# Optimization experiments

Hardware: AMD Instinct MI355X
Metric: run time of the kernel (lower is better)

The kernel has to match this reference:

```python
import jax, jax.numpy as jnp
import numpy as np

N_E, N_C, H = 100000, 50000, 256
D_E, D_C = 768, 1024
E_EE, E_EC, E_CE = 800000, 400000, 400000
EPS = 1e-12


def setup_inputs() -> dict:
    key = jax.random.key(0)
    ks = jax.random.split(key, 16)
    x_entity = jax.random.normal(ks[0], (N_E, D_E), jnp.float32)
    x_chunk = jax.random.normal(ks[1], (N_C, D_C), jnp.float32)
    # edge[0] = source indices, edge[1] = destination indices
    edge_ee = jnp.stack([jax.random.randint(ks[2], (E_EE,), 0, N_E),
                         jax.random.randint(ks[3], (E_EE,), 0, N_E)])
    edge_ec = jnp.stack([jax.random.randint(ks[4], (E_EC,), 0, N_E),
                         jax.random.randint(ks[5], (E_EC,), 0, N_C)])
    edge_ce = jnp.stack([jax.random.randint(ks[6], (E_CE,), 0, N_C),
                         jax.random.randint(ks[7], (E_CE,), 0, N_E)])
    # per-type projection weights (stored [in, out]; y = x @ W)
    P_e = jax.random.normal(ks[8], (D_E, H), jnp.float32) / np.sqrt(D_E).astype(np.float32)
    P_c = jax.random.normal(ks[9], (D_C, H), jnp.float32) / np.sqrt(D_C).astype(np.float32)
    s = np.float32(1.0 / np.sqrt(H))
    # SAGEConv params stacked over the 3 edge types: 0=e->e, 1=e->c, 2=c->e
    Wl1 = jax.random.normal(ks[10], (3, H, H), jnp.float32) * s
    bl1 = jnp.zeros((3, H), jnp.float32)
    Wr1 = jax.random.normal(ks[11], (3, H, H), jnp.float32) * s
    Wl2 = jax.random.normal(ks[12], (3, H, H), jnp.float32) * s
    bl2 = jnp.zeros((3, H), jnp.float32)
    Wr2 = jax.random.normal(ks[13], (3, H, H), jnp.float32) * s
    return {"x_entity": x_entity, "x_chunk": x_chunk,
            "edge_ee": edge_ee, "edge_ec": edge_ec, "edge_ce": edge_ce,
            "P_e": P_e, "P_c": P_c,
            "Wl1": Wl1, "bl1": bl1, "Wr1": Wr1,
            "Wl2": Wl2, "bl2": bl2, "Wr2": Wr2}


def _sage(x_src, x_dst, edge, Wl, bl, Wr, n_dst):
    # PyG SAGEConv: lin_l(mean of neighbor features) + lin_r(x_dst)
    msg = x_src[edge[0]]                                   # [E, H] gather
    agg = jax.ops.segment_sum(msg, edge[1], num_segments=n_dst)
    cnt = jax.ops.segment_sum(jnp.ones((edge.shape[1], 1), x_src.dtype),
                              edge[1], num_segments=n_dst)
    mean = agg / jnp.maximum(cnt, 1.0)                     # isolated nodes -> 0
    return mean @ Wl + bl + x_dst @ Wr


def _l2norm(v):
    # F.normalize(v, dim=1), eps=1e-12
    n = jnp.sqrt(jnp.sum(v * v, axis=1, keepdims=True))
    return v / jnp.maximum(n, EPS)


def reference(x_entity, x_chunk, edge_ee, edge_ec, edge_ce,
              P_e, P_c, Wl1, bl1, Wr1, Wl2, bl2, Wr2):
    # per-type projection (bias=False)
    h_e = x_entity @ P_e
    h_c = x_chunk @ P_c
    id_e, id_c = h_e, h_c
    # conv1: HeteroConv(aggr='sum') -> sum SAGE outputs per destination type
    o_e = (_sage(h_e, h_e, edge_ee, Wl1[0], bl1[0], Wr1[0], N_E)
           + _sage(h_c, h_e, edge_ce, Wl1[2], bl1[2], Wr1[2], N_E))
    o_c = _sage(h_e, h_c, edge_ec, Wl1[1], bl1[1], Wr1[1], N_C)
    # dropout(0.1) is identity in eval; relu then residual
    h_e = jax.nn.relu(o_e) + id_e
    h_c = jax.nn.relu(o_c) + id_c
    # conv2
    o_e = (_sage(h_e, h_e, edge_ee, Wl2[0], bl2[0], Wr2[0], N_E)
           + _sage(h_c, h_e, edge_ce, Wl2[2], bl2[2], Wr2[2], N_E))
    o_c = _sage(h_e, h_c, edge_ec, Wl2[1], bl2[1], Wr2[1], N_C)
    return _l2norm(o_e), _l2norm(o_c)
```

## Files before the change

kernel.cpp:

```cpp
#include <hip/hip_runtime.h>
#include <hip/hip_bf16.h>

#define N_E 100000
#define N_C 50000
#define H 256
#define D_E 768
#define D_C 1024
#define E_EE 800000
#define E_EC 400000
#define E_CE 400000

#define ME_PAD 100096
#define MC_PAD 50048

typedef unsigned short u16;
typedef __attribute__((ext_vector_type(8))) short bf16x8;
typedef __attribute__((ext_vector_type(4))) float f32x4;

__device__ __forceinline__ float bf2f(u16 x) {
    unsigned u = ((unsigned)x) << 16;
    return __builtin_bit_cast(float, u);
}
__device__ __forceinline__ u16 f2bf(float f) {
    unsigned u = __builtin_bit_cast(unsigned, f);
    u = (u + 0x7fffu + ((u >> 16) & 1u)) >> 16;
    return (u16)u;
}

__global__ __launch_bounds__(1024) void transpose_w_k(const float* __restrict__ in,
                                                      u16* __restrict__ out, int K) {
    __shared__ float t[32][33];
    int k0 = blockIdx.x * 32, n0 = blockIdx.y * 32;
    int tx = threadIdx.x, ty = threadIdx.y;
    t[ty][tx] = in[(size_t)(k0 + ty) * H + n0 + tx];
    __syncthreads();
    out[(size_t)(n0 + ty) * K + k0 + tx] = f2bf(t[tx][ty]);
}

__global__ __launch_bounds__(1024) void transpose_wsum_k(const float* __restrict__ a,
                                                         const float* __restrict__ b,
                                                         u16* __restrict__ out) {
    __shared__ float t[32][33];
    int k0 = blockIdx.x * 32, n0 = blockIdx.y * 32;
    int tx = threadIdx.x, ty = threadIdx.y;
    size_t idx = (size_t)(k0 + ty) * H + n0 + tx;
    t[ty][tx] = a[idx] + b[idx];
    __syncthreads();
    out[(size_t)(n0 + ty) * H + k0 + tx] = f2bf(t[tx][ty]);
}

__global__ __launch_bounds__(256) void hist_k(const int* __restrict__ dst, int E,
                                              int* __restrict__ cnt) {
    int i = blockIdx.x * 256 + threadIdx.x;
    if (i < E) atomicAdd(&cnt[dst[i]], 1);
}

#define SCAN_N (2 * N_E + N_C)
#define SCAN_NB ((SCAN_N + 1023) / 1024)

__global__ __launch_bounds__(1024) void scan_blk_k(const int* __restrict__ cnt,
                                                   int* __restrict__ part,
                                                   int* __restrict__ bsum) {
    __shared__ int sm[1024];
    int i = blockIdx.x * 1024 + threadIdx.x;
    int v = (i < SCAN_N) ? cnt[i] : 0;
    sm[threadIdx.x] = v;
    __syncthreads();
    for (int off = 1; off < 1024; off <<= 1) {
        int t = (threadIdx.x >= off) ? sm[threadIdx.x - off] : 0;
        __syncthreads();
        sm[threadIdx.x] += t;
        __syncthreads();
    }
    if (i < SCAN_N) part[i] = sm[threadIdx.x] - v;
    if (threadIdx.x == 1023) bsum[blockIdx.x] = sm[1023];
}

__global__ __launch_bounds__(1024) void scan_top_k(int* __restrict__ bsum) {
    __shared__ int sm[1024];
    int v = (threadIdx.x < SCAN_NB) ? bsum[threadIdx.x] : 0;
    sm[threadIdx.x] = v;
    __syncthreads();
    for (int off = 1; off < 1024; off <<= 1) {
        int t = (threadIdx.x >= off) ? sm[threadIdx.x - off] : 0;
        __syncthreads();
        sm[threadIdx.x] += t;
        __syncthreads();
    }
    if (threadIdx.x < SCAN_NB) bsum[threadIdx.x] = sm[threadIdx.x] - v;
}

__global__ __launch_bounds__(1024) void scan_out_k(const int* __restrict__ part,
                                                   const int* __restrict__ bsum,
                                                   int* __restrict__ eePtr, int* __restrict__ eeCur,
                                                   int* __restrict__ cePtr, int* __restrict__ ceCur,
                                                   int* __restrict__ ecPtr, int* __restrict__ ecCur) {
    int i = blockIdx.x * 1024 + threadIdx.x;
    if (i < SCAN_N) {
        int v = part[i] + bsum[blockIdx.x];
        if (i < N_E) {
            eePtr[i] = v; eeCur[i] = v;
        } else if (i < 2 * N_E) {
            int j = i - N_E, w = v - E_EE;
            cePtr[j] = w; ceCur[j] = w;
        } else {
            int j = i - 2 * N_E, w = v - (E_EE + E_CE);
            ecPtr[j] = w; ecCur[j] = w;
        }
    }
    if (i == 0) {
        eePtr[N_E] = E_EE;
        cePtr[N_E] = E_CE;
        ecPtr[N_C] = E_EC;
    }
}

__global__ __launch_bounds__(256) void reorder_k(const int* __restrict__ src,
                                                 const int* __restrict__ dst, int E,
                                                 int* __restrict__ cursor,
                                                 int* __restrict__ srcSorted) {
    int e = blockIdx.x * 256 + threadIdx.x;
    if (e < E) {
        int pos = atomicAdd(&cursor[dst[e]], 1);
        srcSorted[pos] = src[e];
    }
}

__global__ __launch_bounds__(256) void gather_mean_k(const u16* __restrict__ feat,
                                                     const int* __restrict__ rowptr,
                                                     const int* __restrict__ srcIdx,
                                                     int nDst, int nPad,
                                                     u16* __restrict__ outAgg) {
    int r = blockIdx.x * 4 + (threadIdx.x >> 6);
    if (r >= nPad) return;
    int lane = threadIdx.x & 63;
    float ax = 0.f, ay = 0.f, az = 0.f, aw = 0.f;
    int deg = 0;
    if (r < nDst) {
        int e0 = rowptr[r], e1 = rowptr[r + 1];
        deg = e1 - e0;
        int e = e0;
        for (; e + 1 < e1; e += 2) {
            int s0 = srcIdx[e], s1 = srcIdx[e + 1];
            ushort4 v0 = *reinterpret_cast<const ushort4*>(feat + (size_t)s0 * H + lane * 4);
            ushort4 v1 = *reinterpret_cast<const ushort4*>(feat + (size_t)s1 * H + lane * 4);
            ax += bf2f(v0.x) + bf2f(v1.x);
            ay += bf2f(v0.y) + bf2f(v1.y);
            az += bf2f(v0.z) + bf2f(v1.z);
            aw += bf2f(v0.w) + bf2f(v1.w);
        }
        if (e < e1) {
            int s0 = srcIdx[e];
            ushort4 v0 = *reinterpret_cast<const ushort4*>(feat + (size_t)s0 * H + lane * 4);
            ax += bf2f(v0.x); ay += bf2f(v0.y); az += bf2f(v0.z); aw += bf2f(v0.w);
        }
    }
    float inv = deg > 0 ? 1.f / (float)deg : 0.f;
    ushort4 o;
    o.x = f2bf(ax * inv); o.y = f2bf(ay * inv); o.z = f2bf(az * inv); o.w = f2bf(aw * inv);
    *reinterpret_cast<ushort4*>(outAgg + (size_t)r * H + lane * 4) = o;
}


struct GemmArgs {
    const u16* A[3];
    const u16* Wt[3];
    int K;
    int nPairs;
    const float* bias1;
    const float* bias2;
    const u16* res;
    void* out;
    int Mvalid;
    int mode;
};

__global__ __launch_bounds__(512, 4) void gemm_bf16_k(GemmArgs g) {
    __shared__ char lds[2][24576];
    __shared__ float rowsq[128];
    const int tid = threadIdx.x;
    const int lane = tid & 63;
    const int wid = tid >> 6;
    const int wm = wid >> 2;
    const int wn = wid & 3;
    const int row0 = blockIdx.x * 128;
    const int K = g.K;

    const int srow = tid >> 2;
    const int au = (tid & 3) ^ ((srow >> 1) & 3);
    const int ofsA = (row0 + srow) * K + au * 8;
    const int ofsB1 = srow * K + au * 8;
    const int brow2 = 128 + srow;
    const int bu2 = (tid & 3) ^ ((brow2 >> 1) & 3);
    const int ofsB2 = brow2 * K + bu2 * 8;

    int a_off[4], b_off[4];
#pragma unroll
    for (int mi = 0; mi < 4; ++mi) {
        int row = wm * 64 + mi * 16 + (lane & 15);
        int u = (lane >> 4) ^ ((row >> 1) & 3);
        a_off[mi] = row * 64 + u * 16;
    }
#pragma unroll
    for (int ni = 0; ni < 4; ++ni) {
        int row = wn * 64 + ni * 16 + (lane & 15);
        int u = (lane >> 4) ^ ((row >> 1) & 3);
        b_off[ni] = 8192 + row * 64 + u * 16;
    }

#define STAGE(p_, kk_, ph_)                                                                       \
    do {                                                                                          \
        const u16* A_ = g.A[p_];                                                                  \
        const u16* W_ = g.Wt[p_];                                                                 \
        __builtin_amdgcn_global_load_lds(                                                         \
            (const __attribute__((address_space(1))) void*)(A_ + ofsA + (kk_)),                   \
            (__attribute__((address_space(3))) void*)(lds[ph_] + wid * 1024), 16, 0, 0);          \
        __builtin_amdgcn_global_load_lds(                                                         \
            (const __attribute__((address_space(1))) void*)(W_ + ofsB1 + (kk_)),                  \
            (__attribute__((address_space(3))) void*)(lds[ph_] + 8192 + wid * 1024), 16, 0, 0);   \
        __builtin_amdgcn_global_load_lds(                                                         \
            (const __attribute__((address_space(1))) void*)(W_ + ofsB2 + (kk_)),                  \
            (__attribute__((address_space(3))) void*)(lds[ph_] + 16384 + wid * 1024), 16, 0, 0);  \
    } while (0)

    f32x4 acc[4][4] = {};
    const int T = g.nPairs * (K >> 5);

    STAGE(0, 0, 0);
    int pn = 0, kn = 32;
    if (kn == K) { kn = 0; pn = 1; }

    for (int s = 0; s < T; ++s) {
        const int ph = s & 1;
        if (s + 1 < T) {
            STAGE(pn, kn, ph ^ 1);
            kn += 32;
            if (kn == K) { kn = 0; ++pn; }
            asm volatile("s_waitcnt vmcnt(3)" ::: "memory");
        } else {
            asm volatile("s_waitcnt vmcnt(0)" ::: "memory");
        }
        __builtin_amdgcn_sched_barrier(0);
        __builtin_amdgcn_s_barrier();

        bf16x8 af[4], bfr[4];
#pragma unroll
        for (int mi = 0; mi < 4; ++mi)
            af[mi] = *reinterpret_cast<const bf16x8*>(lds[ph] + a_off[mi]);
#pragma unroll
        for (int ni = 0; ni < 4; ++ni)
            bfr[ni] = *reinterpret_cast<const bf16x8*>(lds[ph] + b_off[ni]);
#pragma unroll
        for (int mi = 0; mi < 4; ++mi)
#pragma unroll
            for (int ni = 0; ni < 4; ++ni)
                acc[mi][ni] = __builtin_amdgcn_mfma_f32_16x16x32_bf16(af[mi], bfr[ni],
                                                                      acc[mi][ni], 0, 0, 0);
        __builtin_amdgcn_sched_barrier(0);
        __builtin_amdgcn_s_barrier();
    }
#undef STAGE

    const int ccol = wn * 64 + (lane & 15);
    const int crow0 = row0 + wm * 64 + ((lane >> 4) << 2);
    float bv[4];
#pragma unroll
    for (int ni = 0; ni < 4; ++ni) {
        int c = ccol + ni * 16;
        float b = 0.f;
        if (g.bias1) b += g.bias1[c];
        if (g.bias2) b += g.bias2[c];
        bv[ni] = b;
    }

    if (g.mode == 1) {
#pragma unroll
        for (int ni = 0; ni < 4; ++ni) {
            int c = ccol + ni * 16;
#pragma unroll
            for (int mi = 0; mi < 4; ++mi) {
#pragma unroll
                for (int j = 0; j < 4; ++j) {
                    int r = crow0 + mi * 16 + j;
                    size_t idx = (size_t)r * H + c;
                    float v = fmaxf(acc[mi][ni][j] + bv[ni], 0.f) + bf2f(g.res[idx]);
                    ((u16*)g.out)[idx] = f2bf(v);
                }
            }
        }
    } else {
        if (tid < 128) rowsq[tid] = 0.f;
        __syncthreads();
#pragma unroll
        for (int mi = 0; mi < 4; ++mi) {
#pragma unroll
            for (int j = 0; j < 4; ++j) {
                float p = 0.f;
#pragma unroll
                for (int ni = 0; ni < 4; ++ni) {
                    float v = acc[mi][ni][j] + bv[ni];
                    p += v * v;
                }
                p += __shfl_xor(p, 1);
                p += __shfl_xor(p, 2);
                p += __shfl_xor(p, 4);
                p += __shfl_xor(p, 8);
                if ((lane & 15) == 0) {
                    int rl = wm * 64 + mi * 16 + ((lane >> 4) << 2) + j;
                    atomicAdd(&rowsq[rl], p);
                }
            }
        }
        __syncthreads();
#pragma unroll
        for (int mi = 0; mi < 4; ++mi) {
#pragma unroll
            for (int j = 0; j < 4; ++j) {
                int rl = wm * 64 + mi * 16 + ((lane >> 4) << 2) + j;
                int r = row0 + rl;
                if (r < g.Mvalid) {
                    float inv = 1.f / fmaxf(sqrtf(rowsq[rl]), 1e-12f);
#pragma unroll
                    for (int ni = 0; ni < 4; ++ni) {
                        int c = ccol + ni * 16;
                        float v = acc[mi][ni][j] + bv[ni];
                        ((float*)g.out)[(size_t)r * H + c] = v * inv;
                    }
                }
            }
        }
    }
}

struct ProjArgs {
    const float* A;
    const u16* Wt;
    int K;
    int M;
    u16* out;
};

__global__ __launch_bounds__(512, 4) void gemm_proj_k(ProjArgs g) {
    __shared__ char lds[2][24576];
    const int tid = threadIdx.x;
    const int lane = tid & 63;
    const int wid = tid >> 6;
    const int wm = wid >> 2;
    const int wn = wid & 3;
    const int row0 = blockIdx.x * 128;
    const int K = g.K;

    const int srow = tid >> 2;
    const int cunit = tid & 3;
    const int aRow = min(row0 + srow, g.M - 1);
    const float* pA = g.A + (size_t)aRow * K + cunit * 8;
    const int aDst = srow * 64 + (cunit ^ ((srow >> 1) & 3)) * 16;

    const int bu1 = cunit ^ ((srow >> 1) & 3);
    const int ofsB1 = srow * K + bu1 * 8;
    const int brow2 = 128 + srow;
    const int bu2 = cunit ^ ((brow2 >> 1) & 3);
    const int ofsB2 = brow2 * K + bu2 * 8;

    int a_off[4], b_off[4];
#pragma unroll
    for (int mi = 0; mi < 4; ++mi) {
        int row = wm * 64 + mi * 16 + (lane & 15);
        int u = (lane >> 4) ^ ((row >> 1) & 3);
        a_off[mi] = row * 64 + u * 16;
    }
#pragma unroll
    for (int ni = 0; ni < 4; ++ni) {
        int row = wn * 64 + ni * 16 + (lane & 15);
        int u = (lane >> 4) ^ ((row >> 1) & 3);
        b_off[ni] = 8192 + row * 64 + u * 16;
    }

#define BSTAGE(kk_, ph_)                                                                          \
    do {                                                                                          \
        __builtin_amdgcn_global_load_lds(                                                         \
            (const __attribute__((address_space(1))) void*)(g.Wt + ofsB1 + (kk_)),               \
            (__attribute__((address_space(3))) void*)(lds[ph_] + 8192 + wid * 1024), 16, 0, 0);   \
        __builtin_amdgcn_global_load_lds(                                                         \
            (const __attribute__((address_space(1))) void*)(g.Wt + ofsB2 + (kk_)),               \
            (__attribute__((address_space(3))) void*)(lds[ph_] + 16384 + wid * 1024), 16, 0, 0);  \
    } while (0)

    f32x4 acc[4][4] = {};
    const int T = K >> 5;

    BSTAGE(0, 0);
    float4 c0 = *reinterpret_cast<const float4*>(pA);
    float4 c1 = *reinterpret_cast<const float4*>(pA + 4);

    for (int s = 0; s < T; ++s) {
        const int ph = s & 1;
        float4 n0 = make_float4(0.f, 0.f, 0.f, 0.f), n1 = n0;
        if (s + 1 < T) {
            BSTAGE((s + 1) * 32, ph ^ 1);
            n0 = *reinterpret_cast<const float4*>(pA + (s + 1) * 32);
            n1 = *reinterpret_cast<const float4*>(pA + (s + 1) * 32 + 4);
        }
        union { bf16x8 v; u16 e[8]; } pk;
        pk.e[0] = f2bf(c0.x); pk.e[1] = f2bf(c0.y); pk.e[2] = f2bf(c0.z); pk.e[3] = f2bf(c0.w);
        pk.e[4] = f2bf(c1.x); pk.e[5] = f2bf(c1.y); pk.e[6] = f2bf(c1.z); pk.e[7] = f2bf(c1.w);
        *reinterpret_cast<bf16x8*>(lds[ph] + aDst) = pk.v;
        asm volatile("s_waitcnt lgkmcnt(0)" ::: "memory");
        __builtin_amdgcn_sched_barrier(0);
        __builtin_amdgcn_s_barrier();

        bf16x8 af[4], bfr[4];
#pragma unroll
        for (int mi = 0; mi < 4; ++mi)
            af[mi] = *reinterpret_cast<const bf16x8*>(lds[ph] + a_off[mi]);
#pragma unroll
        for (int ni = 0; ni < 4; ++ni)
            bfr[ni] = *reinterpret_cast<const bf16x8*>(lds[ph] + b_off[ni]);
#pragma unroll
        for (int mi = 0; mi < 4; ++mi)
#pragma unroll
            for (int ni = 0; ni < 4; ++ni)
                acc[mi][ni] = __builtin_amdgcn_mfma_f32_16x16x32_bf16(af[mi], bfr[ni],
                                                                      acc[mi][ni], 0, 0, 0);
        __builtin_amdgcn_sched_barrier(0);
        __builtin_amdgcn_s_barrier();
        c0 = n0; c1 = n1;
    }
#undef BSTAGE

    const int ccol = wn * 64 + (lane & 15);
    const int crow0 = row0 + wm * 64 + ((lane >> 4) << 2);
#pragma unroll
    for (int ni = 0; ni < 4; ++ni) {
        int c = ccol + ni * 16;
#pragma unroll
        for (int mi = 0; mi < 4; ++mi) {
#pragma unroll
            for (int j = 0; j < 4; ++j) {
                int r = crow0 + mi * 16 + j;
                g.out[(size_t)r * H + c] = f2bf(acc[mi][ni][j]);
            }
        }
    }
}

extern "C" void kernel_launch(void* const* d_in, const int* in_sizes, int n_in,
                              void* d_out, int out_size, void* d_ws, size_t ws_size,
                              hipStream_t stream) {
    const float* x_e = (const float*)d_in[0];
    const float* x_c = (const float*)d_in[1];
    const int* e_ee = (const int*)d_in[2];
    const int* e_ec = (const int*)d_in[3];
    const int* e_ce = (const int*)d_in[4];
    const float* P_e = (const float*)d_in[5];
    const float* P_c = (const float*)d_in[6];
    const float* Wl1 = (const float*)d_in[7];
    const float* bl1 = (const float*)d_in[8];
    const float* Wr1 = (const float*)d_in[9];
    const float* Wl2 = (const float*)d_in[10];
    const float* bl2 = (const float*)d_in[11];
    const float* Wr2 = (const float*)d_in[12];
    float* out = (float*)d_out;

    const size_t EHp = (size_t)ME_PAD * H;
    const size_t CHp = (size_t)MC_PAD * H;

    u16* us = (u16*)d_ws;
    u16* he0 = us;   us += EHp;
    u16* he1 = us;   us += EHp;
    u16* aggE1 = us; us += EHp;
    u16* aggE2 = us; us += EHp;
    u16* hc0 = us;   us += CHp;
    u16* hc1 = us;   us += CHp;
    u16* aggC = us;  us += CHp;
    u16* PeT = us;   us += H * D_E;
    u16* PcT = us;   us += H * D_C;
    u16* WlT1 = us;  us += 3 * H * H;
    u16* WrT1_1 = us; us += H * H;
    u16* WrT1s = us;  us += H * H;
    u16* WlT2 = us;  us += 3 * H * H;
    u16* WrT2_1 = us; us += H * H;
    u16* WrT2s = us;  us += H * H;

    int* ip = (int*)us;
    int* eePtr = ip;  ip += N_E + 1;
    int* eeSrc = ip;  ip += E_EE;
    int* eeCur = ip;  ip += N_E;
    int* cePtr = ip;  ip += N_E + 1;
    int* ceSrc = ip;  ip += E_CE;
    int* ceCur = ip;  ip += N_E;
    int* ecPtr = ip;  ip += N_C + 1;
    int* ecSrc = ip;  ip += E_EC;
    int* ecCur = ip;  ip += N_C;
    int* cntAll = ip; ip += SCAN_N;
    int* part = ip;   ip += SCAN_N;
    int* bsum = ip;   ip += SCAN_NB + 1;

    const int WHH = H * H;

    hipMemsetAsync(cntAll, 0, (size_t)SCAN_N * sizeof(int), stream);
    hist_k<<<(E_EE + 255) / 256, 256, 0, stream>>>(e_ee + E_EE, E_EE, cntAll);
    hist_k<<<(E_CE + 255) / 256, 256, 0, stream>>>(e_ce + E_CE, E_CE, cntAll + N_E);
    hist_k<<<(E_EC + 255) / 256, 256, 0, stream>>>(e_ec + E_EC, E_EC, cntAll + 2 * N_E);
    scan_blk_k<<<SCAN_NB, 1024, 0, stream>>>(cntAll, part, bsum);
    scan_top_k<<<1, 1024, 0, stream>>>(bsum);
    scan_out_k<<<SCAN_NB, 1024, 0, stream>>>(part, bsum, eePtr, eeCur, cePtr, ceCur, ecPtr, ecCur);
    reorder_k<<<(E_EE + 255) / 256, 256, 0, stream>>>(e_ee, e_ee + E_EE, E_EE, eeCur, eeSrc);
    reorder_k<<<(E_CE + 255) / 256, 256, 0, stream>>>(e_ce, e_ce + E_CE, E_CE, ceCur, ceSrc);
    reorder_k<<<(E_EC + 255) / 256, 256, 0, stream>>>(e_ec, e_ec + E_EC, E_EC, ecCur, ecSrc);

    {
        dim3 blk(32, 32);
        transpose_w_k<<<dim3(D_E / 32, H / 32), blk, 0, stream>>>(P_e, PeT, D_E);
        transpose_w_k<<<dim3(D_C / 32, H / 32), blk, 0, stream>>>(P_c, PcT, D_C);
        for (int p = 0; p < 3; ++p) {
            transpose_w_k<<<dim3(H / 32, H / 32), blk, 0, stream>>>(Wl1 + p * WHH, WlT1 + p * WHH, H);
            transpose_w_k<<<dim3(H / 32, H / 32), blk, 0, stream>>>(Wl2 + p * WHH, WlT2 + p * WHH, H);
        }
        transpose_w_k<<<dim3(H / 32, H / 32), blk, 0, stream>>>(Wr1 + 1 * WHH, WrT1_1, H);
        transpose_w_k<<<dim3(H / 32, H / 32), blk, 0, stream>>>(Wr2 + 1 * WHH, WrT2_1, H);
        transpose_wsum_k<<<dim3(H / 32, H / 32), blk, 0, stream>>>(Wr1 + 0 * WHH, Wr1 + 2 * WHH, WrT1s);
        transpose_wsum_k<<<dim3(H / 32, H / 32), blk, 0, stream>>>(Wr2 + 0 * WHH, Wr2 + 2 * WHH, WrT2s);
    }

    const int gridE = ME_PAD / 128, gridC = MC_PAD / 128;

    {
        ProjArgs g{x_e, PeT, D_E, N_E, he0};
        gemm_proj_k<<<gridE, 512, 0, stream>>>(g);
    }
    {
        ProjArgs g{x_c, PcT, D_C, N_C, hc0};
        gemm_proj_k<<<gridC, 512, 0, stream>>>(g);
    }

    gather_mean_k<<<ME_PAD / 4, 256, 0, stream>>>(he0, eePtr, eeSrc, N_E, ME_PAD, aggE1);
    gather_mean_k<<<ME_PAD / 4, 256, 0, stream>>>(hc0, cePtr, ceSrc, N_E, ME_PAD, aggE2);
    gather_mean_k<<<MC_PAD / 4, 256, 0, stream>>>(he0, ecPtr, ecSrc, N_C, MC_PAD, aggC);
    {
        GemmArgs g{};
        g.A[0] = aggE1; g.Wt[0] = WlT1 + 0 * WHH;
        g.A[1] = aggE2; g.Wt[1] = WlT1 + 2 * WHH;
        g.A[2] = he0;   g.Wt[2] = WrT1s;
        g.K = H; g.nPairs = 3;
        g.bias1 = bl1 + 0 * H; g.bias2 = bl1 + 2 * H;
        g.res = he0; g.out = he1; g.mode = 1;
        gemm_bf16_k<<<gridE, 512, 0, stream>>>(g);
    }
    {
        GemmArgs g{};
        g.A[0] = aggC; g.Wt[0] = WlT1 + 1 * WHH;
        g.A[1] = hc0;  g.Wt[1] = WrT1_1;
        g.K = H; g.nPairs = 2;
        g.bias1 = bl1 + 1 * H;
        g.res = hc0; g.out = hc1; g.mode = 1;
        gemm_bf16_k<<<gridC, 512, 0, stream>>>(g);
    }

    gather_mean_k<<<ME_PAD / 4, 256, 0, stream>>>(he1, eePtr, eeSrc, N_E, ME_PAD, aggE1);
    gather_mean_k<<<ME_PAD / 4, 256, 0, stream>>>(hc1, cePtr, ceSrc, N_E, ME_PAD, aggE2);
    gather_mean_k<<<MC_PAD / 4, 256, 0, stream>>>(he1, ecPtr, ecSrc, N_C, MC_PAD, aggC);
    {
        GemmArgs g{};
        g.A[0] = aggE1; g.Wt[0] = WlT2 + 0 * WHH;
        g.A[1] = aggE2; g.Wt[1] = WlT2 + 2 * WHH;
        g.A[2] = he1;   g.Wt[2] = WrT2s;
        g.K = H; g.nPairs = 3;
        g.bias1 = bl2 + 0 * H; g.bias2 = bl2 + 2 * H;
        g.out = out; g.Mvalid = N_E; g.mode = 2;
        gemm_bf16_k<<<gridE, 512, 0, stream>>>(g);
    }
    {
        GemmArgs g{};
        g.A[0] = aggC; g.Wt[0] = WlT2 + 1 * WHH;
        g.A[1] = hc1;  g.Wt[1] = WrT2_1;
        g.K = H; g.nPairs = 2;
        g.bias1 = bl2 + 1 * H;
        g.out = out + (size_t)N_E * H; g.Mvalid = N_C; g.mode = 2;
        gemm_bf16_k<<<gridC, 512, 0, stream>>>(g);
    }
}
```

Measured before the change: 982.4 us.

## Batch per-edge-type kernels into single launches and widen gather loads

Merges the three histogram, reorder and gather launches, the two projection GEMMs, the paired conv GEMMs and the twelve weight transposes into one grouped launch each, with the job chosen from the block index. This cuts launch count and the tail idle time between small kernels. The gather also moves from 8-byte to 16-byte loads, with two half-wavefronts working on different edges and combining their sums through a cross-lane shuffle. Packing the indices into one combined cursor/source buffer adds some per-thread branching, and the transpose grid launches idle blocks for the smaller jobs.

New measurement: 893.4 us. 9.1% less time.

```diff
diff --git a/kernel.cpp b/kernel.cpp
--- a/kernel.cpp
+++ b/kernel.cpp
@@ -9,6 +9,7 @@
 #define E_EE 800000
 #define E_EC 400000
 #define E_CE 400000
+#define E_TOT (E_EE + E_CE + E_EC)
 
 #define ME_PAD 100096
 #define MC_PAD 50048
@@ -27,32 +28,38 @@
     return (u16)u;
 }
 
-__global__ __launch_bounds__(1024) void transpose_w_k(const float* __restrict__ in,
-                                                      u16* __restrict__ out, int K) {
-    __shared__ float t[32][33];
-    int k0 = blockIdx.x * 32, n0 = blockIdx.y * 32;
-    int tx = threadIdx.x, ty = threadIdx.y;
-    t[ty][tx] = in[(size_t)(k0 + ty) * H + n0 + tx];
-    __syncthreads();
-    out[(size_t)(n0 + ty) * K + k0 + tx] = f2bf(t[tx][ty]);
-}
-
-__global__ __launch_bounds__(1024) void transpose_wsum_k(const float* __restrict__ a,
-                                                         const float* __restrict__ b,
-                                                         u16* __restrict__ out) {
-    __shared__ float t[32][33];
-    int k0 = blockIdx.x * 32, n0 = blockIdx.y * 32;
+struct TransJobs {
+    const float* a[12];
+    const float* b[12];
+    u16* dst[12];
+    int K[12];
+};
+
+__global__ __launch_bounds__(1024) void transpose_all_k(TransJobs t) {
+    int j = blockIdx.z;
+    int K = t.K[j];
+    int k0 = blockIdx.x * 32;
+    if (k0 >= K) return;
+    int n0 = blockIdx.y * 32;
+    __shared__ float sm[32][33];
     int tx = threadIdx.x, ty = threadIdx.y;
     size_t idx = (size_t)(k0 + ty) * H + n0 + tx;
-    t[ty][tx] = a[idx] + b[idx];
+    float v = t.a[j][idx];
+    if (t.b[j]) v += t.b[j][idx];
+    sm[ty][tx] = v;
     __syncthreads();
-    out[(size_t)(n0 + ty) * H + k0 + tx] = f2bf(t[tx][ty]);
-}
-
-__global__ __launch_bounds__(256) void hist_k(const int* __restrict__ dst, int E,
-                                              int* __restrict__ cnt) {
+    t.dst[j][(size_t)(n0 + ty) * K + k0 + tx] = f2bf(sm[tx][ty]);
+}
+
+__global__ __launch_bounds__(256) void hist3_k(const int* __restrict__ eeD,
+                                               const int* __restrict__ ceD,
+                                               const int* __restrict__ ecD,
+                                               int* __restrict__ cnt) {
     int i = blockIdx.x * 256 + threadIdx.x;
-    if (i < E) atomicAdd(&cnt[dst[i]], 1);
+    if (i >= E_TOT) return;
+    if (i < E_EE) atomicAdd(&cnt[eeD[i]], 1);
+    else if (i < E_EE + E_CE) atomicAdd(&cnt[N_E + ceD[i - E_EE]], 1);
+    else atomicAdd(&cnt[2 * N_E + ecD[i - E_EE - E_CE]], 1);
 }
 
 #define SCAN_N (2 * N_E + N_C)
@@ -92,21 +99,22 @@
 
 __global__ __launch_bounds__(1024) void scan_out_k(const int* __restrict__ part,
                                                    const int* __restrict__ bsum,
-                                                   int* __restrict__ eePtr, int* __restrict__ eeCur,
-                                                   int* __restrict__ cePtr, int* __restrict__ ceCur,
-                                                   int* __restrict__ ecPtr, int* __restrict__ ecCur) {
+                                                   int* __restrict__ eePtr,
+                                                   int* __restrict__ cePtr,
+                                                   int* __restrict__ ecPtr,
+                                                   int* __restrict__ curAll) {
     int i = blockIdx.x * 1024 + threadIdx.x;
     if (i < SCAN_N) {
         int v = part[i] + bsum[blockIdx.x];
+        int w;
         if (i < N_E) {
-            eePtr[i] = v; eeCur[i] = v;
+            w = v; eePtr[i] = w;
         } else if (i < 2 * N_E) {
-            int j = i - N_E, w = v - E_EE;
-            cePtr[j] = w; ceCur[j] = w;
+            w = v - E_EE; cePtr[i - N_E] = w;
         } else {
-            int j = i - 2 * N_E, w = v - (E_EE + E_CE);
-            ecPtr[j] = w; ecCur[j] = w;
-        }
+            w = v - (E_EE + E_CE); ecPtr[i - 2 * N_E] = w;
+        }
+        curAll[i] = w;
     }
     if (i == 0) {
         eePtr[N_E] = E_EE;
@@ -115,57 +123,100 @@
     }
 }
 
-__global__ __launch_bounds__(256) void reorder_k(const int* __restrict__ src,
-                                                 const int* __restrict__ dst, int E,
-                                                 int* __restrict__ cursor,
-                                                 int* __restrict__ srcSorted) {
-    int e = blockIdx.x * 256 + threadIdx.x;
-    if (e < E) {
-        int pos = atomicAdd(&cursor[dst[e]], 1);
-        srcSorted[pos] = src[e];
-    }
-}
-
-__global__ __launch_bounds__(256) void gather_mean_k(const u16* __restrict__ feat,
-                                                     const int* __restrict__ rowptr,
-                                                     const int* __restrict__ srcIdx,
-                                                     int nDst, int nPad,
-                                                     u16* __restrict__ outAgg) {
-    int r = blockIdx.x * 4 + (threadIdx.x >> 6);
-    if (r >= nPad) return;
-    int lane = threadIdx.x & 63;
-    float ax = 0.f, ay = 0.f, az = 0.f, aw = 0.f;
+__global__ __launch_bounds__(256) void reorder3_k(const int* __restrict__ eeS, const int* __restrict__ eeD,
+                                                  const int* __restrict__ ceS, const int* __restrict__ ceD,
+                                                  const int* __restrict__ ecS, const int* __restrict__ ecD,
+                                                  int* __restrict__ curAll, int* __restrict__ srcAll) {
+    int i = blockIdx.x * 256 + threadIdx.x;
+    if (i >= E_TOT) return;
+    if (i < E_EE) {
+        int pos = atomicAdd(&curAll[eeD[i]], 1);
+        srcAll[pos] = eeS[i];
+    } else if (i < E_EE + E_CE) {
+        int k = i - E_EE;
+        int pos = atomicAdd(&curAll[N_E + ceD[k]], 1);
+        srcAll[E_EE + pos] = ceS[k];
+    } else {
+        int k = i - E_EE - E_CE;
+        int pos = atomicAdd(&curAll[2 * N_E + ecD[k]], 1);
+        srcAll[E_EE + E_CE + pos] = ecS[k];
+    }
+}
+
+struct GatherArgs {
+    const u16* feat[3];
+    const int* rowptr[3];
+    const int* srcIdx[3];
+    u16* outAgg[3];
+    int nDst[3];
+    int blkEnd[3];
+};
+
+__device__ __forceinline__ void acc8(float* a, uint4 v) {
+    a[0] += __builtin_bit_cast(float, v.x << 16);
+    a[1] += __builtin_bit_cast(float, v.x & 0xffff0000u);
+    a[2] += __builtin_bit_cast(float, v.y << 16);
+    a[3] += __builtin_bit_cast(float, v.y & 0xffff0000u);
+    a[4] += __builtin_bit_cast(float, v.z << 16);
+    a[5] += __builtin_bit_cast(float, v.z & 0xffff0000u);
+    a[6] += __builtin_bit_cast(float, v.w << 16);
+    a[7] += __builtin_bit_cast(float, v.w & 0xffff0000u);
+}
+
+__global__ __launch_bounds__(256) void gather3_k(GatherArgs a) {
+    const int b = blockIdx.x;
+    const int j = (b >= a.blkEnd[0]) + (b >= a.blkEnd[1]);
+    const int b0 = j ? a.blkEnd[j - 1] : 0;
+    const int r = (b - b0) * 4 + (threadIdx.x >> 6);
+    const int lane = threadIdx.x & 63;
+    const int half = lane >> 5;
+    const int pos = lane & 31;
+
+    float acc[8] = {};
     int deg = 0;
-    if (r < nDst) {
-        int e0 = rowptr[r], e1 = rowptr[r + 1];
+    if (r < a.nDst[j]) {
+        const int* __restrict__ rp = a.rowptr[j];
+        const int* __restrict__ si = a.srcIdx[j];
+        const u16* __restrict__ ft = a.feat[j];
+        int e0 = rp[r], e1 = rp[r + 1];
         deg = e1 - e0;
         int e = e0;
+        for (; e + 3 < e1; e += 4) {
+            int sA = si[e + half];
+            int sB = si[e + 2 + half];
+            uint4 vA = *(const uint4*)(ft + (size_t)sA * H + pos * 8);
+            uint4 vB = *(const uint4*)(ft + (size_t)sB * H + pos * 8);
+            acc8(acc, vA);
+            acc8(acc, vB);
+        }
         for (; e + 1 < e1; e += 2) {
-            int s0 = srcIdx[e], s1 = srcIdx[e + 1];
-            ushort4 v0 = *reinterpret_cast<const ushort4*>(feat + (size_t)s0 * H + lane * 4);
-            ushort4 v1 = *reinterpret_cast<const ushort4*>(feat + (size_t)s1 * H + lane * 4);
-            ax += bf2f(v0.x) + bf2f(v1.x);
-            ay += bf2f(v0.y) + bf2f(v1.y);
-            az += bf2f(v0.z) + bf2f(v1.z);
-            aw += bf2f(v0.w) + bf2f(v1.w);
-        }
-        if (e < e1) {
-            int s0 = srcIdx[e];
-            ushort4 v0 = *reinterpret_cast<const ushort4*>(feat + (size_t)s0 * H + lane * 4);
-            ax += bf2f(v0.x); ay += bf2f(v0.y); az += bf2f(v0.z); aw += bf2f(v0.w);
-        }
-    }
-    float inv = deg > 0 ? 1.f / (float)deg : 0.f;
-    ushort4 o;
-    o.x = f2bf(ax * inv); o.y = f2bf(ay * inv); o.z = f2bf(az * inv); o.w = f2bf(aw * inv);
-    *reinterpret_cast<ushort4*>(outAgg + (size_t)r * H + lane * 4) = o;
-}
-
-
-struct GemmArgs {
+            int s = si[e + half];
+            uint4 v = *(const uint4*)(ft + (size_t)s * H + pos * 8);
+            acc8(acc, v);
+        }
+        if (e < e1 && half == 0) {
+            int s = si[e];
+            uint4 v = *(const uint4*)(ft + (size_t)s * H + pos * 8);
+            acc8(acc, v);
+        }
+    }
+#pragma unroll
+    for (int k = 0; k < 8; ++k) acc[k] += __shfl_xor(acc[k], 32);
+
+    if (half == 0) {
+        float inv = deg > 0 ? 1.f / (float)deg : 0.f;
+        uint4 o;
+        o.x = (unsigned)f2bf(acc[0] * inv) | ((unsigned)f2bf(acc[1] * inv) << 16);
+        o.y = (unsigned)f2bf(acc[2] * inv) | ((unsigned)f2bf(acc[3] * inv) << 16);
+        o.z = (unsigned)f2bf(acc[4] * inv) | ((unsigned)f2bf(acc[5] * inv) << 16);
+        o.w = (unsigned)f2bf(acc[6] * inv) | ((unsigned)f2bf(acc[7] * inv) << 16);
+        *(uint4*)(a.outAgg[j] + (size_t)r * H + pos * 8) = o;
+    }
+}
+
+struct GemmCfg {
     const u16* A[3];
     const u16* Wt[3];
-    int K;
     int nPairs;
     const float* bias1;
     const float* bias2;
@@ -174,8 +225,16 @@
     int Mvalid;
     int mode;
 };
-
-__global__ __launch_bounds__(512, 4) void gemm_bf16_k(GemmArgs g) {
+struct ConvArgs2 {
+    GemmCfg c[2];
+    int blkSplit;
+};
+
+__global__ __launch_bounds__(512, 4) void gemm_conv_k(ConvArgs2 gg) {
+    const int which = blockIdx.x >= gg.blkSplit;
+    const GemmCfg* __restrict__ g = which ? &gg.c[1] : &gg.c[0];
+    const int row0 = (blockIdx.x - (which ? gg.blkSplit : 0)) * 128;
+
     __shared__ char lds[2][24576];
     __shared__ float rowsq[128];
     const int tid = threadIdx.x;
@@ -183,16 +242,14 @@
     const int wid = tid >> 6;
     const int wm = wid >> 2;
     const int wn = wid & 3;
-    const int row0 = blockIdx.x * 128;
-    const int K = g.K;
 
     const int srow = tid >> 2;
     const int au = (tid & 3) ^ ((srow >> 1) & 3);
-    const int ofsA = (row0 + srow) * K + au * 8;
-    const int ofsB1 = srow * K + au * 8;
+    const int ofsA = (row0 + srow) * H + au * 8;
+    const int ofsB1 = srow * H + au * 8;
     const int brow2 = 128 + srow;
     const int bu2 = (tid & 3) ^ ((brow2 >> 1) & 3);
-    const int ofsB2 = brow2 * K + bu2 * 8;
+    const int ofsB2 = brow2 * H + bu2 * 8;
 
     int a_off[4], b_off[4];
 #pragma unroll
@@ -210,8 +267,8 @@
 
 #define STAGE(p_, kk_, ph_)                                                                       \
     do {                                                                                          \
-        const u16* A_ = g.A[p_];                                                                  \
-        const u16* W_ = g.Wt[p_];                                                                 \
+        const u16* A_ = g->A[p_];                                                                 \
+        const u16* W_ = g->Wt[p_];                                                                \
         __builtin_amdgcn_global_load_lds(                                                         \
             (const __attribute__((address_space(1))) void*)(A_ + ofsA + (kk_)),                   \
             (__attribute__((address_space(3))) void*)(lds[ph_] + wid * 1024), 16, 0, 0);          \
@@ -224,18 +281,18 @@
     } while (0)
 
     f32x4 acc[4][4] = {};
-    const int T = g.nPairs * (K >> 5);
+    const int T = g->nPairs * (H >> 5);
 
     STAGE(0, 0, 0);
     int pn = 0, kn = 32;
-    if (kn == K) { kn = 0; pn = 1; }
+    if (kn == H) { kn = 0; pn = 1; }
 
     for (int s = 0; s < T; ++s) {
         const int ph = s & 1;
         if (s + 1 < T) {
             STAGE(pn, kn, ph ^ 1);
             kn += 32;
-            if (kn == K) { kn = 0; ++pn; }
+            if (kn == H) { kn = 0; ++pn; }
             asm volatile("s_waitcnt vmcnt(3)" ::: "memory");
         } else {
             asm volatile("s_waitcnt vmcnt(0)" ::: "memory");
@@ -268,12 +325,12 @@
     for (int ni = 0; ni < 4; ++ni) {
         int c = ccol + ni * 16;
         float b = 0.f;
-        if (g.bias1) b += g.bias1[c];
-        if (g.bias2) b += g.bias2[c];
+        if (g->bias1) b += g->bias1[c];
+        if (g->bias2) b += g->bias2[c];
         bv[ni] = b;
     }
 
-    if (g.mode == 1) {
+    if (g->mode == 1) {
 #pragma unroll
         for (int ni = 0; ni < 4; ++ni) {
             int c = ccol + ni * 16;
@@ -283,8 +340,8 @@
                 for (int j = 0; j < 4; ++j) {
                     int r = crow0 + mi * 16 + j;
                     size_t idx = (size_t)r * H + c;
-                    float v = fmaxf(acc[mi][ni][j] + bv[ni], 0.f) + bf2f(g.res[idx]);
-                    ((u16*)g.out)[idx] = f2bf(v);
+                    float v = fmaxf(acc[mi][ni][j] + bv[ni], 0.f) + bf2f(g->res[idx]);
+                    ((u16*)g->out)[idx] = f2bf(v);
                 }
             }
         }
@@ -318,13 +375,13 @@
             for (int j = 0; j < 4; ++j) {
                 int rl = wm * 64 + mi * 16 + ((lane >> 4) << 2) + j;
                 int r = row0 + rl;
-                if (r < g.Mvalid) {
+                if (r < g->Mvalid) {
                     float inv = 1.f / fmaxf(sqrtf(rowsq[rl]), 1e-12f);
 #pragma unroll
                     for (int ni = 0; ni < 4; ++ni) {
                         int c = ccol + ni * 16;
                         float v = acc[mi][ni][j] + bv[ni];
-                        ((float*)g.out)[(size_t)r * H + c] = v * inv;
+                        ((float*)g->out)[(size_t)r * H + c] = v * inv;
                     }
                 }
             }
@@ -332,28 +389,35 @@
     }
 }
 
-struct ProjArgs {
-    const float* A;
-    const u16* Wt;
-    int K;
-    int M;
-    u16* out;
+struct ProjArgs2 {
+    const float* A[2];
+    const u16* Wt[2];
+    int K[2];
+    int M[2];
+    u16* out[2];
+    int blkSplit;
 };
 
-__global__ __launch_bounds__(512, 4) void gemm_proj_k(ProjArgs g) {
+__global__ __launch_bounds__(512, 4) void gemm_proj_k(ProjArgs2 gg) {
+    const int which = blockIdx.x >= gg.blkSplit;
+    const int row0 = (blockIdx.x - (which ? gg.blkSplit : 0)) * 128;
+    const float* __restrict__ Aptr = gg.A[which];
+    const u16* __restrict__ Wt = gg.Wt[which];
+    const int K = gg.K[which];
+    const int M = gg.M[which];
+    u16* __restrict__ outp = gg.out[which];
+
     __shared__ char lds[2][24576];
     const int tid = threadIdx.x;
     const int lane = tid & 63;
     const int wid = tid >> 6;
     const int wm = wid >> 2;
     const int wn = wid & 3;
-    const int row0 = blockIdx.x * 128;
-    const int K = g.K;
 
     const int srow = tid >> 2;
     const int cunit = tid & 3;
-    const int aRow = min(row0 + srow, g.M - 1);
-    const float* pA = g.A + (size_t)aRow * K + cunit * 8;
+    const int aRow = min(row0 + srow, M - 1);
+    const float* pA = Aptr + (size_t)aRow * K + cunit * 8;
     const int aDst = srow * 64 + (cunit ^ ((srow >> 1) & 3)) * 16;
 
     const int bu1 = cunit ^ ((srow >> 1) & 3);
@@ -379,10 +443,10 @@
 #define BSTAGE(kk_, ph_)                                                                          \
     do {                                                                                          \
         __builtin_amdgcn_global_load_lds(                                                         \
-            (const __attribute__((address_space(1))) void*)(g.Wt + ofsB1 + (kk_)),               \
+            (const __attribute__((address_space(1))) void*)(Wt + ofsB1 + (kk_)),                  \
             (__attribute__((address_space(3))) void*)(lds[ph_] + 8192 + wid * 1024), 16, 0, 0);   \
         __builtin_amdgcn_global_load_lds(                                                         \
-            (const __attribute__((address_space(1))) void*)(g.Wt + ofsB2 + (kk_)),               \
+            (const __attribute__((address_space(1))) void*)(Wt + ofsB2 + (kk_)),                  \
             (__attribute__((address_space(3))) void*)(lds[ph_] + 16384 + wid * 1024), 16, 0, 0);  \
     } while (0)
 
@@ -438,7 +502,7 @@
 #pragma unroll
             for (int j = 0; j < 4; ++j) {
                 int r = crow0 + mi * 16 + j;
-                g.out[(size_t)r * H + c] = f2bf(acc[mi][ni][j]);
+                outp[(size_t)r * H + c] = f2bf(acc[mi][ni][j]);
             }
         }
     }
@@ -484,14 +548,10 @@
 
     int* ip = (int*)us;
     int* eePtr = ip;  ip += N_E + 1;
-    int* eeSrc = ip;  ip += E_EE;
-    int* eeCur = ip;  ip += N_E;
     int* cePtr = ip;  ip += N_E + 1;
-    int* ceSrc = ip;  ip += E_CE;
-    int* ceCur = ip;  ip += N_E;
     int* ecPtr = ip;  ip += N_C + 1;
-    int* ecSrc = ip;  ip += E_EC;
-    int* ecCur = ip;  ip += N_C;
+    int* curAll = ip; ip += SCAN_N;
+    int* srcAll = ip; ip += E_TOT;
     int* cntAll = ip; ip += SCAN_N;
     int* part = ip;   ip += SCAN_N;
     int* bsum = ip;   ip += SCAN_NB + 1;
@@ -499,84 +559,93 @@
     const int WHH = H * H;
 
     hipMemsetAsync(cntAll, 0, (size_t)SCAN_N * sizeof(int), stream);
-    hist_k<<<(E_EE + 255) / 256, 256, 0, stream>>>(e_ee + E_EE, E_EE, cntAll);
-    hist_k<<<(E_CE + 255) / 256, 256, 0, stream>>>(e_ce + E_CE, E_CE, cntAll + N_E);
-    hist_k<<<(E_EC + 255) / 256, 256, 0, stream>>>(e_ec + E_EC, E_EC, cntAll + 2 * N_E);
+    hist3_k<<<(E_TOT + 255) / 256, 256, 0, stream>>>(e_ee + E_EE, e_ce + E_CE, e_ec + E_EC, cntAll);
     scan_blk_k<<<SCAN_NB, 1024, 0, stream>>>(cntAll, part, bsum);
     scan_top_k<<<1, 1024, 0, stream>>>(bsum);
-    scan_out_k<<<SCAN_NB, 1024, 0, stream>>>(part, bsum, eePtr, eeCur, cePtr, ceCur, ecPtr, ecCur);
-    reorder_k<<<(E_EE + 255) / 256, 256, 0, stream>>>(e_ee, e_ee + E_EE, E_EE, eeCur, eeSrc);
-    reorder_k<<<(E_CE + 255) / 256, 256, 0, stream>>>(e_ce, e_ce + E_CE, E_CE, ceCur, ceSrc);
-    reorder_k<<<(E_EC + 255) / 256, 256, 0, stream>>>(e_ec, e_ec + E_EC, E_EC, ecCur, ecSrc);
+    scan_out_k<<<SCAN_NB, 1024, 0, stream>>>(part, bsum, eePtr, cePtr, ecPtr, curAll);
+    reorder3_k<<<(E_TOT + 255) / 256, 256, 0, stream>>>(e_ee, e_ee + E_EE, e_ce, e_ce + E_CE,
+                                                        e_ec, e_ec + E_EC, curAll, srcAll);
+    const int* eeSrc = srcAll;
+    const int* ceSrc = srcAll + E_EE;
+    const int* ecSrc = srcAll + E_EE + E_CE;
 
     {
-        dim3 blk(32, 32);
-        transpose_w_k<<<dim3(D_E / 32, H / 32), blk, 0, stream>>>(P_e, PeT, D_E);
-        transpose_w_k<<<dim3(D_C / 32, H / 32), blk, 0, stream>>>(P_c, PcT, D_C);
-        for (int p = 0; p < 3; ++p) {
-            transpose_w_k<<<dim3(H / 32, H / 32), blk, 0, stream>>>(Wl1 + p * WHH, WlT1 + p * WHH, H);
-            transpose_w_k<<<dim3(H / 32, H / 32), blk, 0, stream>>>(Wl2 + p * WHH, WlT2 + p * WHH, H);
-        }
-        transpose_w_k<<<dim3(H / 32, H / 32), blk, 0, stream>>>(Wr1 + 1 * WHH, WrT1_1, H);
-        transpose_w_k<<<dim3(H / 32, H / 32), blk, 0, stream>>>(Wr2 + 1 * WHH, WrT2_1, H);
-        transpose_wsum_k<<<dim3(H / 32, H / 32), blk, 0, stream>>>(Wr1 + 0 * WHH, Wr1 + 2 * WHH, WrT1s);
-        transpose_wsum_k<<<dim3(H / 32, H / 32), blk, 0, stream>>>(Wr2 + 0 * WHH, Wr2 + 2 * WHH, WrT2s);
+        TransJobs t{};
+        int n = 0;
+        auto add = [&](const float* a, const float* b, u16* d, int K) {
+            t.a[n] = a; t.b[n] = b; t.dst[n] = d; t.K[n] = K; ++n;
+        };
+        add(P_e, nullptr, PeT, D_E);
+        add(P_c, nullptr, PcT, D_C);
+        for (int p = 0; p < 3; ++p) add(Wl1 + p * WHH, nullptr, WlT1 + p * WHH, H);
+        for (int p = 0; p < 3; ++p) add(Wl2 + p * WHH, nullptr, WlT2 + p * WHH, H);
+        add(Wr1 + 1 * WHH, nullptr, WrT1_1, H);
+        add(Wr2 + 1 * WHH, nullptr, WrT2_1, H);
+        add(Wr1 + 0 * WHH, Wr1 + 2 * WHH, WrT1s, H);
+        add(Wr2 + 0 * WHH, Wr2 + 2 * WHH, WrT2s, H);
+        transpose_all_k<<<dim3(D_C / 32, H / 32, 12), dim3(32, 32), 0, stream>>>(t);
     }
 
     const int gridE = ME_PAD / 128, gridC = MC_PAD / 128;
 
     {
-        ProjArgs g{x_e, PeT, D_E, N_E, he0};
-        gemm_proj_k<<<gridE, 512, 0, stream>>>(g);
-    }
+        ProjArgs2 g{};
+        g.A[0] = x_e; g.Wt[0] = PeT; g.K[0] = D_E; g.M[0] = N_E; g.out[0] = he0;
+        g.A[1] = x_c; g.Wt[1] = PcT; g.K[1] = D_C; g.M[1] = N_C; g.out[1] = hc0;
+        g.blkSplit = gridE;
+        gemm_proj_k<<<gridE + gridC, 512, 0, stream>>>(g);
+    }
+
+    const int gBlkE = ME_PAD / 4, gBlkC = MC_PAD / 4;
+    const int gTotal = 2 * gBlkE + gBlkC;
+
     {
-        ProjArgs g{x_c, PcT, D_C, N_C, hc0};
-        gemm_proj_k<<<gridC, 512, 0, stream>>>(g);
-    }
-
-    gather_mean_k<<<ME_PAD / 4, 256, 0, stream>>>(he0, eePtr, eeSrc, N_E, ME_PAD, aggE1);
-    gather_mean_k<<<ME_PAD / 4, 256, 0, stream>>>(hc0, cePtr, ceSrc, N_E, ME_PAD, aggE2);
-    gather_mean_k<<<MC_PAD / 4, 256, 0, stream>>>(he0, ecPtr, ecSrc, N_C, MC_PAD, aggC);
+        GatherArgs a{};
+        a.feat[0] = he0; a.rowptr[0] = eePtr; a.srcIdx[0] = eeSrc; a.outAgg[0] = aggE1; a.nDst[0] = N_E;
+        a.feat[1] = hc0; a.rowptr[1] = cePtr; a.srcIdx[1] = ceSrc; a.outAgg[1] = aggE2; a.nDst[1] = N_E;
+        a.feat[2] = he0; a.rowptr[2] = ecPtr; a.srcIdx[2] = ecSrc; a.outAgg[2] = aggC;  a.nDst[2] = N_C;
+        a.blkEnd[0] = gBlkE; a.blkEnd[1] = 2 * gBlkE; a.blkEnd[2] = gTotal;
+        gather3_k<<<gTotal, 256, 0, stream>>>(a);
+    }
     {
-        GemmArgs g{};
-        g.A[0] = aggE1; g.Wt[0] = WlT1 + 0 * WHH;
-        g.A[1] = aggE2; g.Wt[1] = WlT1 + 2 * WHH;
-        g.A[2] = he0;   g.Wt[2] = WrT1s;
-        g.K = H; g.nPairs = 3;
-        g.bias1 = bl1 + 0 * H; g.bias2 = bl1 + 2 * H;
-        g.res = he0; g.out = he1; g.mode = 1;
-        gemm_bf16_k<<<gridE, 512, 0, stream>>>(g);
-    }
+        ConvArgs2 g{};
+        g.c[0].A[0] = aggE1; g.c[0].Wt[0] = WlT1 + 0 * WHH;
+        g.c[0].A[1] = aggE2; g.c[0].Wt[1] = WlT1 + 2 * WHH;
+        g.c[0].A[2] = he0;   g.c[0].Wt[2] = WrT1s;
+        g.c[0].nPairs = 3;
+        g.c[0].bias1 = bl1 + 0 * H; g.c[0].bias2 = bl1 + 2 * H;
+        g.c[0].res = he0; g.c[0].out = he1; g.c[0].mode = 1;
+        g.c[1].A[0] = aggC; g.c[1].Wt[0] = WlT1 + 1 * WHH;
+        g.c[1].A[1] = hc0;  g.c[1].Wt[1] = WrT1_1;
+        g.c[1].nPairs = 2;
+        g.c[1].bias1 = bl1 + 1 * H;
+        g.c[1].res = hc0; g.c[1].out = hc1; g.c[1].mode = 1;
+        g.blkSplit = gridE;
+        gemm_conv_k<<<gridE + gridC, 512, 0, stream>>>(g);
+    }
+
     {
-        GemmArgs g{};
-        g.A[0] = aggC; g.Wt[0] = WlT1 + 1 * WHH;
-        g.A[1] = hc0;  g.Wt[1] = WrT1_1;
-        g.K = H; g.nPairs = 2;
-        g.bias1 = bl1 + 1 * H;
-        g.res = hc0; g.out = hc1; g.mode = 1;
-        gemm_bf16_k<<<gridC, 512, 0, stream>>>(g);
-    }
-
-    gather_mean_k<<<ME_PAD / 4, 256, 0, stream>>>(he1, eePtr, eeSrc, N_E, ME_PAD, aggE1);
-    gather_mean_k<<<ME_PAD / 4, 256, 0, stream>>>(hc1, cePtr, ceSrc, N_E, ME_PAD, aggE2);
-    gather_mean_k<<<MC_PAD / 4, 256, 0, stream>>>(he1, ecPtr, ecSrc, N_C, MC_PAD, aggC);
+        GatherArgs a{};
+        a.feat[0] = he1; a.rowptr[0] = eePtr; a.srcIdx[0] = eeSrc; a.outAgg[0] = aggE1; a.nDst[0] = N_E;
+        a.feat[1] = hc1; a.rowptr[1] = cePtr; a.srcIdx[1] = ceSrc; a.outAgg[1] = aggE2; a.nDst[1] = N_E;
+        a.feat[2] = he1; a.rowptr[2] = ecPtr; a.srcIdx[2] = ecSrc; a.outAgg[2] = aggC;  a.nDst[2] = N_C;
+        a.blkEnd[0] = gBlkE; a.blkEnd[1] = 2 * gBlkE; a.blkEnd[2] = gTotal;
+        gather3_k<<<gTotal, 256, 0, stream>>>(a);
+    }
     {
-        GemmArgs g{};
-        g.A[0] = aggE1; g.Wt[0] = WlT2 + 0 * WHH;
-        g.A[1] = aggE2; g.Wt[1] = WlT2 + 2 * WHH;
-        g.A[2] = he1;   g.Wt[2] = WrT2s;
-        g.K = H; g.nPairs = 3;
-        g.bias1 = bl2 + 0 * H; g.bias2 = bl2 + 2 * H;
-        g.out = out; g.Mvalid = N_E; g.mode = 2;
-        gemm_bf16_k<<<gridE, 512, 0, stream>>>(g);
-    }
-    {
-        GemmArgs g{};
-        g.A[0] = aggC; g.Wt[0] = WlT2 + 1 * WHH;
-        g.A[1] = hc1;  g.Wt[1] = WrT2_1;
-        g.K = H; g.nPairs = 2;
-        g.bias1 = bl2 + 1 * H;
-        g.out = out + (size_t)N_E * H; g.Mvalid = N_C; g.mode = 2;
-        gemm_bf16_k<<<gridC, 512, 0, stream>>>(g);
-    }
-}
+        ConvArgs2 g{};
+        g.c[0].A[0] = aggE1; g.c[0].Wt[0] = WlT2 + 0 * WHH;
+        g.c[0].A[1] = aggE2; g.c[0].Wt[1] = WlT2 + 2 * WHH;
+        g.c[0].A[2] = he1;   g.c[0].Wt[2] = WrT2s;
+        g.c[0].nPairs = 3;
+        g.c[0].bias1 = bl2 + 0 * H; g.c[0].bias2 = bl2 + 2 * H;
+        g.c[0].out = out; g.c[0].Mvalid = N_E; g.c[0].mode = 2;
+        g.c[1].A[0] = aggC; g.c[1].Wt[0] = WlT2 + 1 * WHH;
+        g.c[1].A[1] = hc1;  g.c[1].Wt[1] = WrT2_1;
+        g.c[1].nPairs = 2;
+        g.c[1].bias1 = bl2 + 1 * H;
+        g.c[1].out = out + (size_t)N_E * H; g.c[1].Mvalid = N_C; g.c[1].mode = 2;
+        g.blkSplit = gridE;
+        gemm_conv_k<<<gridE + gridC, 512, 0, stream>>>(g);
+    }
+}
```
